# Optimization experiments

Measured on AMD Instinct MI355X. Metric: run time of the kernel, lower is better.

Reference implementation:

```python
import jax, jax.numpy as jnp
import numpy as np

N_NODES = 100000
N_FEAT = 512
HIDDEN = 64
N_CLASSES = 40
N_EDGES = 3200000
K = 10
ALPHA = 0.1


def setup_inputs() -> dict:
    key = jax.random.key(0)
    k1, k2, k3, k4 = jax.random.split(key, 4)
    x = jax.random.normal(k1, (N_NODES, N_FEAT), dtype=jnp.float32)
    # Glorot-ish scaled linear weights
    W1 = jax.random.normal(k2, (N_FEAT, HIDDEN), dtype=jnp.float32) / np.sqrt(N_FEAT)
    b1 = jnp.zeros((HIDDEN,), dtype=jnp.float32)
    W2 = jax.random.normal(k3, (HIDDEN, N_CLASSES), dtype=jnp.float32) / np.sqrt(HIDDEN)
    b2 = jnp.zeros((N_CLASSES,), dtype=jnp.float32)
    edge_index = jax.random.randint(k4, (2, N_EDGES), 0, N_NODES, dtype=jnp.int64)
    return {"x": x, "W1": W1, "b1": b1, "W2": W2, "b2": b2, "edge_index": edge_index}


def reference(x, W1, b1, W2, b2, edge_index):
    n = x.shape[0]
    # MLP (dropout is identity in eval mode)
    h = jnp.maximum(x @ W1 + b1, 0.0)
    h = h @ W2 + b2  # [N, C]

    # gcn_norm with self-loops: A_hat = D^{-1/2} (A + I) D^{-1/2}
    loops = jnp.arange(n, dtype=edge_index.dtype)
    row = jnp.concatenate([edge_index[0], loops])  # source (gather)
    col = jnp.concatenate([edge_index[1], loops])  # target (scatter)
    deg = jax.ops.segment_sum(jnp.ones(row.shape, dtype=h.dtype), col, num_segments=n)
    dinv = jnp.where(deg > 0, jax.lax.rsqrt(deg), 0.0)
    norm = dinv[row] * dinv[col]  # [E + N]

    h0 = h

    def step(z, _):
        msg = norm[:, None] * z[row]                      # gather + scale
        agg = jax.ops.segment_sum(msg, col, num_segments=n)  # scatter-add
        z = ALPHA * h0 + (1.0 - ALPHA) * agg
        return z, None

    z, _ = jax.lax.scan(step, h0, None, length=K)
    return jax.nn.log_softmax(z, axis=1)
```

## Files before the change

### kernel.cpp

```cpp
#include <hip/hip_runtime.h>
#include <hip/hip_bf16.h>
#include <hip/hip_fp16.h>

#define N_NODES   100000
#define N_FEAT    512
#define HIDDEN    64
#define N_CLASSES 40
#define KITER     10
#define ALPHA     0.1f
#define ZP        64
#define HPITCH    72
#define NXCD      8
#define WIN       (N_NODES / NXCD)
#define SUBCAP    65536
#define PARTB     2048
#define CAP       384

typedef __attribute__((ext_vector_type(8))) short bf16x8;
typedef __attribute__((ext_vector_type(4))) float f32x4;

__device__ __forceinline__ float bf2f(unsigned short u) {
    union { unsigned int i; float f; } c;
    c.i = ((unsigned int)u) << 16;
    return c.f;
}
__device__ __forceinline__ unsigned short f2bf(float f) {
    union { float f; unsigned int u; } c; c.f = f;
    unsigned int r = c.u + 0x7FFFu + ((c.u >> 16) & 1u);
    return (unsigned short)(r >> 16);
}

__global__ void zero_flags_kernel(int* __restrict__ flags) {
    if (threadIdx.x < 2) flags[threadIdx.x] = 0;
}

__global__ void detect_float_kernel(const unsigned short* __restrict__ w1raw,
                                    int* __restrict__ flags) {
    int i = blockIdx.x * blockDim.x + threadIdx.x;
    if (i < 32768) {
        unsigned short u = w1raw[i];
        if ((u & 0x7F80u) == 0x7F80u) atomicAdd(&flags[0], 1);
    }
}

__global__ void detect_edge_kernel(const int* __restrict__ ei, int* __restrict__ flags) {
    int i = blockIdx.x * blockDim.x + threadIdx.x;
    if (i < 2048) {
        if (ei[2 * i + 1] != 0) atomicAdd(&flags[1], 1);
    }
}

__global__ void pack_w1_kernel(const void* __restrict__ W1p, const int* __restrict__ flags,
                               unsigned short* __restrict__ pb) {
    int idx = blockIdx.x * 256 + threadIdx.x;
    int j    = idx & 7;
    int lane = (idx >> 3) & 63;
    int ktnt = idx >> 9;
    int kt = ktnt & 15, nt = ktnt >> 4;
    int k = kt * 32 + (lane >> 4) * 8 + j;
    int n = nt * 16 + (lane & 15);
    unsigned short v;
    if (flags[0] > 0) v = f2bf(((const float*)W1p)[k * HIDDEN + n]);
    else              v = ((const unsigned short*)W1p)[k * HIDDEN + n];
    pb[idx] = v;
}

__global__ void pack_w2_kernel(const void* __restrict__ W2p, const int* __restrict__ flags,
                               unsigned short* __restrict__ pb2) {
    int idx = blockIdx.x * 256 + threadIdx.x;
    if (idx >= 3072) return;
    int j    = idx & 7;
    int lane = (idx >> 3) & 63;
    int ktnt = idx >> 9;
    int kt = ktnt & 1, nt = ktnt >> 1;
    int k = kt * 32 + (lane >> 4) * 8 + j;
    int n = nt * 16 + (lane & 15);
    unsigned short v = 0;
    if (n < N_CLASSES) {
        if (flags[0] > 0) v = f2bf(((const float*)W2p)[k * N_CLASSES + n]);
        else              v = ((const unsigned short*)W2p)[k * N_CLASSES + n];
    }
    pb2[idx] = v;
}

__global__ __launch_bounds__(256) void mlp_kernel(
    const void* __restrict__ xp,
    const unsigned short* __restrict__ pb,
    const unsigned short* __restrict__ pb2,
    const void* __restrict__ b1p,
    const void* __restrict__ b2p,
    const int* __restrict__ flags,
    const float* __restrict__ dinv,
    float* __restrict__ h0,
    __half* __restrict__ zh0)
{
    __shared__ unsigned short hsb[16 * HPITCH];
    const int t    = threadIdx.x;
    const int wave = t >> 6;
    const int lane = t & 63;
    const int quad = lane >> 4;
    const int ml   = lane & 15;
    const int base = blockIdx.x * 16;
    const int isf32 = flags[0] > 0;

    const bf16x8* pbv = (const bf16x8*)pb;

    f32x4 acc = {0.f, 0.f, 0.f, 0.f};
    if (!isf32) {
        const unsigned short* xrow = (const unsigned short*)xp
                                   + (size_t)(base + ml) * N_FEAT + quad * 8;
        #pragma unroll
        for (int kt = 0; kt < 16; ++kt) {
            bf16x8 a = *(const bf16x8*)(xrow + kt * 32);
            bf16x8 b = pbv[(wave * 16 + kt) * 64 + lane];
            acc = __builtin_amdgcn_mfma_f32_16x16x32_bf16(a, b, acc, 0, 0, 0);
        }
    } else {
        const float* xf = (const float*)xp + (size_t)(base + ml) * N_FEAT + quad * 8;
        #pragma unroll
        for (int kt = 0; kt < 16; ++kt) {
            float4 lo = *(const float4*)(xf + kt * 32);
            float4 hi = *(const float4*)(xf + kt * 32 + 4);
            bf16x8 a;
            a[0] = (short)f2bf(lo.x); a[1] = (short)f2bf(lo.y);
            a[2] = (short)f2bf(lo.z); a[3] = (short)f2bf(lo.w);
            a[4] = (short)f2bf(hi.x); a[5] = (short)f2bf(hi.y);
            a[6] = (short)f2bf(hi.z); a[7] = (short)f2bf(hi.w);
            bf16x8 b = pbv[(wave * 16 + kt) * 64 + lane];
            acc = __builtin_amdgcn_mfma_f32_16x16x32_bf16(a, b, acc, 0, 0, 0);
        }
    }

    float b1v = isf32 ? ((const float*)b1p)[wave * 16 + ml]
                      : bf2f(((const unsigned short*)b1p)[wave * 16 + ml]);
    #pragma unroll
    for (int r = 0; r < 4; ++r)
        hsb[(quad * 4 + r) * HPITCH + wave * 16 + ml] = f2bf(fmaxf(acc[r] + b1v, 0.0f));
    __syncthreads();

    if (wave < 3) {
        const bf16x8* pb2v = (const bf16x8*)pb2;
        f32x4 acc2 = {0.f, 0.f, 0.f, 0.f};
        #pragma unroll
        for (int kt = 0; kt < 2; ++kt) {
            bf16x8 a = *(const bf16x8*)(hsb + ml * HPITCH + kt * 32 + quad * 8);
            bf16x8 b = pb2v[(wave * 2 + kt) * 64 + lane];
            acc2 = __builtin_amdgcn_mfma_f32_16x16x32_bf16(a, b, acc2, 0, 0, 0);
        }
        int n = wave * 16 + ml;
        if (n < N_CLASSES) {
            float b2v = isf32 ? ((const float*)b2p)[n] : bf2f(((const unsigned short*)b2p)[n]);
            #pragma unroll
            for (int r = 0; r < 4; ++r) {
                int node = base + quad * 4 + r;
                float v = acc2[r] + b2v;
                h0[(size_t)node * N_CLASSES + n] = v;
                zh0[(size_t)node * ZP + n] = __float2half(v * dinv[node]);
            }
        }
    }
}

__global__ void zero_cnt_kernel(int* __restrict__ cnt, int* __restrict__ cur) {
    int i = blockIdx.x * blockDim.x + threadIdx.x;
    if (i < N_NODES) cnt[i] = 0;
    if (i < 65) cur[i] = 0;
}

__global__ void dinv_kernel(const int* __restrict__ cnt, float* __restrict__ dinv) {
    int i = blockIdx.x * blockDim.x + threadIdx.x;
    if (i < N_NODES) dinv[i] = rsqrtf((float)cnt[i] + 1.0f);
}

__global__ void zero_pad_kernel(__half* __restrict__ a, __half* __restrict__ b) {
    int t = threadIdx.x;
    if (t < ZP)            a[(size_t)N_NODES * ZP + t]        = __float2half(0.0f);
    else if (t < 2 * ZP)   b[(size_t)N_NODES * ZP + (t - ZP)] = __float2half(0.0f);
}

__global__ __launch_bounds__(1024) void scan_kernel(
    const int* __restrict__ cnt, int* __restrict__ rptr, int* __restrict__ wpos, int E)
{
    __shared__ int wsum[16];
    __shared__ int carry_s, tiletot_s;
    const int t = threadIdx.x, wave = t >> 6, lane = t & 63;
    if (t == 0) carry_s = 0;
    __syncthreads();
    for (int base = 0; base < N_NODES; base += 4096) {
        int i0 = base + t * 4;
        int v0 = (i0 + 0 < N_NODES) ? cnt[i0 + 0] : 0;
        int v1 = (i0 + 1 < N_NODES) ? cnt[i0 + 1] : 0;
        int v2 = (i0 + 2 < N_NODES) ? cnt[i0 + 2] : 0;
        int v3 = (i0 + 3 < N_NODES) ? cnt[i0 + 3] : 0;
        int tl = v0 + v1 + v2 + v3;
        int sc = tl;
        #pragma unroll
        for (int off = 1; off < 64; off <<= 1) {
            int u = __shfl_up(sc, off, 64);
            if (lane >= off) sc += u;
        }
        if (lane == 63) wsum[wave] = sc;
        int wexcl = sc - tl;
        __syncthreads();
        if (wave == 0) {
            int wv = (lane < 16) ? wsum[lane] : 0;
            int ws = wv;
            #pragma unroll
            for (int off = 1; off < 16; off <<= 1) {
                int u = __shfl_up(ws, off, 64);
                if (lane >= off) ws += u;
            }
            if (lane < 16) wsum[lane] = ws - wv;
            if (lane == 15) tiletot_s = ws;
        }
        __syncthreads();
        int P  = carry_s + wsum[wave] + wexcl;
        int e0 = P, e1 = P + v0, e2 = e1 + v1, e3 = e2 + v2;
        if (i0 + 0 < N_NODES) { rptr[i0 + 0] = e0; wpos[i0 + 0] = e0; }
        if (i0 + 1 < N_NODES) { rptr[i0 + 1] = e1; wpos[i0 + 1] = e1; }
        if (i0 + 2 < N_NODES) { rptr[i0 + 2] = e2; wpos[i0 + 2] = e2; }
        if (i0 + 3 < N_NODES) { rptr[i0 + 3] = e3; wpos[i0 + 3] = e3; }
        __syncthreads();
        if (t == 0) carry_s += tiletot_s;
        __syncthreads();
    }
    if (t == 0) rptr[N_NODES] = E;
}

__global__ __launch_bounds__(256) void partition_kernel(
    const int* __restrict__ ei, const int* __restrict__ flags,
    int* __restrict__ cnt, unsigned int* __restrict__ sub,
    int* __restrict__ cur, int2* __restrict__ ovf, int E)
{
    __shared__ unsigned buf[NXCD][CAP];
    __shared__ int cnt_lds[NXCD];
    __shared__ unsigned base_s[NXCD];

    const int i64f = flags[1] == 0;
    const int xcd  = blockIdx.x & 7;
    const int per  = (E + PARTB - 1) / PARTB;
    const int e0   = blockIdx.x * per;
    const int e1   = min(e0 + per, E);

    if (threadIdx.x < NXCD) cnt_lds[threadIdx.x] = 0;
    __syncthreads();

    for (int e = e0 + threadIdx.x; e < e1; e += 256) {
        int c = i64f ? __builtin_nontemporal_load(ei + 2 * E + 2 * e)
                     : __builtin_nontemporal_load(ei + E + e);
        int r = i64f ? __builtin_nontemporal_load(ei + 2 * e)
                     : __builtin_nontemporal_load(ei + e);
        atomicAdd(&cnt[c], 1);
        int w = c / WIN;
        unsigned pk = (unsigned)r | ((unsigned)(c - w * WIN) << 17);
        int slot = atomicAdd(&cnt_lds[w], 1);
        if (slot < CAP) buf[w][slot] = pk;
        else { int op = atomicAdd(cur + 64, 1); ovf[op] = make_int2(r, c); }
    }
    __syncthreads();

    const int g   = threadIdx.x >> 5;
    const int l32 = threadIdx.x & 31;
    const int n   = min(cnt_lds[g], CAP);
    if (l32 == 0 && n > 0) base_s[g] = (unsigned)atomicAdd(&cur[g * 8 + xcd], n);
    __syncthreads();
    if (n > 0) {
        unsigned base = base_s[g];
        unsigned bslot = (unsigned)(g * 8 + xcd) * SUBCAP;
        for (int i = l32; i < n; i += 32) {
            unsigned p = base + (unsigned)i;
            unsigned pk = buf[g][i];
            if (p < SUBCAP) sub[bslot + p] = pk;
            else {
                int op = atomicAdd(cur + 64, 1);
                ovf[op] = make_int2((int)(pk & 0x1FFFFu), g * WIN + (int)(pk >> 17));
            }
        }
    }
}

__global__ __launch_bounds__(256) void scatter_kernel(
    const unsigned int* __restrict__ sub, const int* __restrict__ cur,
    const int2* __restrict__ ovf,
    int* __restrict__ wpos, int* __restrict__ srcidx)
{
    const int w = blockIdx.x & 7;
    const int tid64 = (blockIdx.x >> 3) * 256 + threadIdx.x;
    int P[9];
    P[0] = 0;
    #pragma unroll
    for (int a = 0; a < 8; ++a) {
        int na = cur[w * 8 + a];
        na = na > SUBCAP ? SUBCAP : na;
        P[a + 1] = P[a] + na;
    }
    const int total = P[8];
    for (int v = tid64; v < total; v += 65536) {
        int a = 0;
        #pragma unroll
        for (int q = 1; q < 8; ++q) if (v >= P[q]) a = q;
        unsigned pk = sub[(unsigned)(w * 8 + a) * SUBCAP + (v - P[a])];
        int r = (int)(pk & 0x1FFFFu);
        int c = w * WIN + (int)(pk >> 17);
        int pos = atomicAdd(&wpos[c], 1);
        srcidx[pos] = r;
    }
    int ov = cur[64];
    for (int i = tid64; i < ov; i += 65536) {
        int2 rc = ovf[i];
        if (rc.y / WIN == w) {
            int pos = atomicAdd(&wpos[rc.y], 1);
            srcidx[pos] = rc.x;
        }
    }
}

__global__ __launch_bounds__(256) void prop_kernel(
    const __half* __restrict__ zh, const float* __restrict__ h0,
    const float* __restrict__ dinv, const int* __restrict__ rptr,
    const int* __restrict__ srcidx, __half* __restrict__ zout)
{
    const int wave = threadIdx.x >> 6;
    const int lane = threadIdx.x & 63;
    const int g    = lane >> 4;
    const int l    = lane & 15;
    const int node = blockIdx.x * 16 + wave * 4 + g;
    const int c0   = l * 4;

    const int beg = rptr[node];
    const int end = rptr[node + 1];
    int nch = (end - beg + 15) >> 4;
    int m1    = max(nch, __shfl_xor(nch, 16, 64));
    int maxch = max(m1,  __shfl_xor(m1, 32, 64));

    float di = dinv[node];
    uint2 yself = *(const uint2*)(zh + ((size_t)node << 6) + c0);
    float h00 = 0.f, h01 = 0.f, h02 = 0.f, h03 = 0.f;
    if (c0 < N_CLASSES) {
        const float* hp = h0 + (size_t)node * N_CLASSES + c0;
        h00 = hp[0]; h01 = hp[1]; h02 = hp[2]; h03 = hp[3];
    }

    float a0 = 0.f, a1 = 0.f, a2 = 0.f, a3 = 0.f;
    float b0 = 0.f, b1 = 0.f, b2 = 0.f, b3 = 0.f;

    for (int ch = 0; ch < maxch; ++ch) {
        int idx = beg + ch * 16 + l;
        int sw  = (idx < end) ? srcidx[idx] : N_NODES;

        #pragma unroll
        for (int i = 0; i < 16; i += 2) {
            int s0 = __shfl(sw, (g << 4) + i,     64);
            int s1 = __shfl(sw, (g << 4) + i + 1, 64);
            uint2 z0 = *(const uint2*)(zh + ((size_t)s0 << 6) + c0);
            uint2 z1 = *(const uint2*)(zh + ((size_t)s1 << 6) + c0);
            const __half2* p0 = (const __half2*)&z0;
            const __half2* p1 = (const __half2*)&z1;
            float2 f00 = __half22float2(p0[0]);
            float2 f01 = __half22float2(p0[1]);
            float2 f10 = __half22float2(p1[0]);
            float2 f11 = __half22float2(p1[1]);
            a0 += f00.x; a1 += f00.y; a2 += f01.x; a3 += f01.y;
            b0 += f10.x; b1 += f10.y; b2 += f11.x; b3 += f11.y;
        }
    }

    if (c0 < N_CLASSES) {
        const __half2* ps = (const __half2*)&yself;
        float2 s01 = __half22float2(ps[0]);
        float2 s23 = __half22float2(ps[1]);
        float kk = (1.0f - ALPHA) * di;
        float o0 = ALPHA * h00 + kk * (a0 + b0 + s01.x);
        float o1 = ALPHA * h01 + kk * (a1 + b1 + s01.y);
        float o2 = ALPHA * h02 + kk * (a2 + b2 + s23.x);
        float o3 = ALPHA * h03 + kk * (a3 + b3 + s23.y);
        __half2 q01 = __floats2half2_rn(di * o0, di * o1);
        __half2 q23 = __floats2half2_rn(di * o2, di * o3);
        uint2 st;
        st.x = *(unsigned int*)&q01;
        st.y = *(unsigned int*)&q23;
        *(uint2*)(zout + ((size_t)node << 6) + c0) = st;
    }
}

__global__ __launch_bounds__(256) void lsm_kernel(
    const __half* __restrict__ zh, const float* __restrict__ dinv,
    const int* __restrict__ flags, void* __restrict__ outp)
{
    const int wave = threadIdx.x >> 6;
    const int lane = threadIdx.x & 63;
    const int node = blockIdx.x * 4 + wave;
    const int isf32 = flags[0] > 0;

    float di = dinv[node];
    float v = (lane < N_CLASSES)
            ? __half2float(zh[(size_t)node * ZP + lane]) / di : -1e30f;
    float m = v;
    #pragma unroll
    for (int o = 32; o; o >>= 1) m = fmaxf(m, __shfl_xor(m, o, 64));
    float e = (lane < N_CLASSES) ? expf(v - m) : 0.0f;
    float s = e;
    #pragma unroll
    for (int o = 32; o; o >>= 1) s += __shfl_xor(s, o, 64);
    float ls = logf(s);
    if (lane < N_CLASSES) {
        float r = v - m - ls;
        size_t idx = (size_t)node * N_CLASSES + lane;
        if (isf32) ((float*)outp)[idx] = r;
        else       ((__hip_bfloat16*)outp)[idx] = __float2bfloat16(r);
    }
}

extern "C" void kernel_launch(void* const* d_in, const int* in_sizes, int n_in,
                              void* d_out, int out_size, void* d_ws, size_t ws_size,
                              hipStream_t stream)
{
    const void* x  = d_in[0];
    const void* W1 = d_in[1];
    const void* b1 = d_in[2];
    const void* W2 = d_in[3];
    const void* b2 = d_in[4];
    const int* ei = (const int*)d_in[5];
    const int E = in_sizes[5] / 2;

    char* ws = (char*)d_ws;
    size_t off = 0;
    auto carve = [&](size_t bytes) -> void* {
        void* p = ws + off;
        off = (off + bytes + 255) & ~(size_t)255;
        return p;
    };
    float*  h0    = (float*) carve((size_t)N_NODES * N_CLASSES * 4);
    __half* zhA   = (__half*)carve((size_t)(N_NODES + 1) * ZP * 2);
    __half* zhB   = (__half*)carve((size_t)(N_NODES + 1) * ZP * 2);
    int*    cnt   = (int*)   carve((size_t)N_NODES * 4);
    float*  dinv  = (float*) carve((size_t)N_NODES * 4);
    int*    rptr  = (int*)   carve((size_t)(N_NODES + 1) * 4);
    int*    wpos  = (int*)   carve((size_t)N_NODES * 4);
    int*    srcidx= (int*)   carve((size_t)E * 4);
    unsigned int* sub = (unsigned int*)carve((size_t)64 * SUBCAP * 4);
    int*    cur   = (int*)   carve(65 * sizeof(int));
    unsigned short* pb  = (unsigned short*)carve(32768 * 2);
    unsigned short* pb2 = (unsigned short*)carve(3072 * 2);
    int*    flags = (int*)   carve(2 * sizeof(int));
    (void)ws_size; (void)n_in; (void)out_size;

    int2* ovf = (int2*)zhA;

    const int nodeBlocks = N_NODES / 4;
    const int mlpBlocks  = N_NODES / 16;
    const int propBlocks = N_NODES / 16;
    const int nThreads1  = (N_NODES + 255) / 256;

    zero_flags_kernel<<<1, 64, 0, stream>>>(flags);
    detect_float_kernel<<<128, 256, 0, stream>>>((const unsigned short*)W1, flags);
    detect_edge_kernel<<<8, 256, 0, stream>>>(ei, flags);
    pack_w1_kernel<<<128, 256, 0, stream>>>(W1, flags, pb);
    pack_w2_kernel<<<12, 256, 0, stream>>>(W2, flags, pb2);

    zero_cnt_kernel<<<nThreads1, 256, 0, stream>>>(cnt, cur);
    partition_kernel<<<PARTB, 256, 0, stream>>>(ei, flags, cnt, sub, cur, ovf, E);
    dinv_kernel<<<nThreads1, 256, 0, stream>>>(cnt, dinv);
    scan_kernel<<<1, 1024, 0, stream>>>(cnt, rptr, wpos, E);
    scatter_kernel<<<2048, 256, 0, stream>>>(sub, cur, ovf, wpos, srcidx);
    zero_pad_kernel<<<1, 128, 0, stream>>>(zhA, zhB);

    mlp_kernel<<<mlpBlocks, 256, 0, stream>>>(x, pb, pb2, b1, b2, flags, dinv, h0, zhA);

    const __half* zin = zhA;
    __half* zout = zhB;
    const __half* zlast = zhA;
    for (int it = 0; it < KITER; ++it) {
        prop_kernel<<<propBlocks, 256, 0, stream>>>(zin, h0, dinv, rptr, srcidx, zout);
        zlast = zout;
        zin = zout;
        zout = (zout == zhB) ? zhA : zhB;
    }

    lsm_kernel<<<nodeBlocks, 256, 0, stream>>>(zlast, dinv, flags, d_out);
}
```

Before: 1.250 ms.

## Replace global-atomic degree count and scatter with per-bucket LDS histograms

Drops the global atomicAdd on cnt in the partition pass. Degrees are now computed from per-subbucket LDS histograms of the packed edge buckets, and cnt_kernel reduces those histograms into cnt and dinv. The scatter pass uses LDS cursors seeded from rptr plus prefix histograms instead of global atomics on wpos. This trades millions of global atomics for an extra read pass over sub and only 64 blocks of 1024 threads, which may underuse the GPU in hist and scatter.

```diff
diff --git a/kernel.cpp b/kernel.cpp
--- a/kernel.cpp
+++ b/kernel.cpp
@@ -30,8 +30,10 @@
     return (unsigned short)(r >> 16);
 }
 
-__global__ void zero_flags_kernel(int* __restrict__ flags) {
-    if (threadIdx.x < 2) flags[threadIdx.x] = 0;
+__global__ void zero_cur_kernel(int* __restrict__ cur, int* __restrict__ flags) {
+    int t = threadIdx.x;
+    if (t < 65) cur[t] = 0;
+    if (t >= 65 && t < 67) flags[t - 65] = 0;
 }
 
 __global__ void detect_float_kernel(const unsigned short* __restrict__ w1raw,
@@ -161,25 +163,103 @@
     }
 }
 
-__global__ void zero_cnt_kernel(int* __restrict__ cnt, int* __restrict__ cur) {
-    int i = blockIdx.x * blockDim.x + threadIdx.x;
-    if (i < N_NODES) cnt[i] = 0;
-    if (i < 65) cur[i] = 0;
-}
-
-__global__ void dinv_kernel(const int* __restrict__ cnt, float* __restrict__ dinv) {
-    int i = blockIdx.x * blockDim.x + threadIdx.x;
-    if (i < N_NODES) dinv[i] = rsqrtf((float)cnt[i] + 1.0f);
-}
-
 __global__ void zero_pad_kernel(__half* __restrict__ a, __half* __restrict__ b) {
     int t = threadIdx.x;
     if (t < ZP)            a[(size_t)N_NODES * ZP + t]        = __float2half(0.0f);
     else if (t < 2 * ZP)   b[(size_t)N_NODES * ZP + (t - ZP)] = __float2half(0.0f);
 }
 
+__global__ __launch_bounds__(256) void partition_kernel(
+    const int* __restrict__ ei, const int* __restrict__ flags,
+    unsigned int* __restrict__ sub,
+    int* __restrict__ cur, int2* __restrict__ ovf, int E)
+{
+    __shared__ unsigned buf[NXCD][CAP];
+    __shared__ int cnt_lds[NXCD];
+    __shared__ unsigned base_s[NXCD];
+
+    const int i64f = flags[1] == 0;
+    const int xcd  = blockIdx.x & 7;
+    const int per  = (E + PARTB - 1) / PARTB;
+    const int e0   = blockIdx.x * per;
+    const int e1   = min(e0 + per, E);
+
+    if (threadIdx.x < NXCD) cnt_lds[threadIdx.x] = 0;
+    __syncthreads();
+
+    for (int e = e0 + threadIdx.x; e < e1; e += 256) {
+        int c = i64f ? __builtin_nontemporal_load(ei + 2 * E + 2 * e)
+                     : __builtin_nontemporal_load(ei + E + e);
+        int r = i64f ? __builtin_nontemporal_load(ei + 2 * e)
+                     : __builtin_nontemporal_load(ei + e);
+        int w = c / WIN;
+        unsigned pk = (unsigned)r | ((unsigned)(c - w * WIN) << 17);
+        int slot = atomicAdd(&cnt_lds[w], 1);
+        if (slot < CAP) buf[w][slot] = pk;
+        else { int op = atomicAdd(cur + 64, 1); ovf[op] = make_int2(r, c); }
+    }
+    __syncthreads();
+
+    const int g   = threadIdx.x >> 5;
+    const int l32 = threadIdx.x & 31;
+    const int n   = min(cnt_lds[g], CAP);
+    if (l32 == 0 && n > 0) base_s[g] = (unsigned)atomicAdd(&cur[g * 8 + xcd], n);
+    __syncthreads();
+    if (n > 0) {
+        unsigned base = base_s[g];
+        unsigned bslot = (unsigned)(g * 8 + xcd) * SUBCAP;
+        for (int i = l32; i < n; i += 32) {
+            unsigned p = base + (unsigned)i;
+            unsigned pk = buf[g][i];
+            if (p < SUBCAP) sub[bslot + p] = pk;
+            else {
+                int op = atomicAdd(cur + 64, 1);
+                ovf[op] = make_int2((int)(pk & 0x1FFFFu), g * WIN + (int)(pk >> 17));
+            }
+        }
+    }
+}
+
+__global__ __launch_bounds__(1024) void hist_kernel(
+    const unsigned int* __restrict__ sub, const int* __restrict__ cur,
+    const int2* __restrict__ ovf, int* __restrict__ hists)
+{
+    __shared__ int h[WIN];
+    const int w = blockIdx.x & 7;
+    const int s = blockIdx.x >> 3;
+    for (int off = threadIdx.x; off < WIN; off += 1024) h[off] = 0;
+    __syncthreads();
+    int n = min(cur[w * 8 + s], SUBCAP);
+    const unsigned int* sp = sub + (size_t)(w * 8 + s) * SUBCAP;
+    for (int i = threadIdx.x; i < n; i += 1024)
+        atomicAdd(&h[sp[i] >> 17], 1);
+    if (s == 7) {
+        int ov = cur[64];
+        for (int i = threadIdx.x; i < ov; i += 1024) {
+            int2 rc = ovf[i];
+            int ww = rc.y / WIN;
+            if (ww == w) atomicAdd(&h[rc.y - ww * WIN], 1);
+        }
+    }
+    __syncthreads();
+    for (int off = threadIdx.x; off < WIN; off += 1024)
+        hists[(size_t)(w * 8 + s) * WIN + off] = h[off];
+}
+
+__global__ void cnt_kernel(const int* __restrict__ hists, int* __restrict__ cnt,
+                           float* __restrict__ dinv) {
+    int i = blockIdx.x * 256 + threadIdx.x;
+    if (i >= N_NODES) return;
+    int w = i / WIN, off = i - w * WIN;
+    int c = 0;
+    #pragma unroll
+    for (int x = 0; x < 8; ++x) c += hists[(size_t)(w * 8 + x) * WIN + off];
+    cnt[i] = c;
+    dinv[i] = rsqrtf((float)c + 1.0f);
+}
+
 __global__ __launch_bounds__(1024) void scan_kernel(
-    const int* __restrict__ cnt, int* __restrict__ rptr, int* __restrict__ wpos, int E)
+    const int* __restrict__ cnt, int* __restrict__ rptr, int E)
 {
     __shared__ int wsum[16];
     __shared__ int carry_s, tiletot_s;
@@ -215,11 +295,10 @@
         }
         __syncthreads();
         int P  = carry_s + wsum[wave] + wexcl;
-        int e0 = P, e1 = P + v0, e2 = e1 + v1, e3 = e2 + v2;
-        if (i0 + 0 < N_NODES) { rptr[i0 + 0] = e0; wpos[i0 + 0] = e0; }
-        if (i0 + 1 < N_NODES) { rptr[i0 + 1] = e1; wpos[i0 + 1] = e1; }
-        if (i0 + 2 < N_NODES) { rptr[i0 + 2] = e2; wpos[i0 + 2] = e2; }
-        if (i0 + 3 < N_NODES) { rptr[i0 + 3] = e3; wpos[i0 + 3] = e3; }
+        if (i0 + 0 < N_NODES) rptr[i0 + 0] = P;
+        if (i0 + 1 < N_NODES) rptr[i0 + 1] = P + v0;
+        if (i0 + 2 < N_NODES) rptr[i0 + 2] = P + v0 + v1;
+        if (i0 + 3 < N_NODES) rptr[i0 + 3] = P + v0 + v1 + v2;
         __syncthreads();
         if (t == 0) carry_s += tiletot_s;
         __syncthreads();
@@ -227,90 +306,37 @@
     if (t == 0) rptr[N_NODES] = E;
 }
 
-__global__ __launch_bounds__(256) void partition_kernel(
-    const int* __restrict__ ei, const int* __restrict__ flags,
-    int* __restrict__ cnt, unsigned int* __restrict__ sub,
-    int* __restrict__ cur, int2* __restrict__ ovf, int E)
-{
-    __shared__ unsigned buf[NXCD][CAP];
-    __shared__ int cnt_lds[NXCD];
-    __shared__ unsigned base_s[NXCD];
-
-    const int i64f = flags[1] == 0;
-    const int xcd  = blockIdx.x & 7;
-    const int per  = (E + PARTB - 1) / PARTB;
-    const int e0   = blockIdx.x * per;
-    const int e1   = min(e0 + per, E);
-
-    if (threadIdx.x < NXCD) cnt_lds[threadIdx.x] = 0;
-    __syncthreads();
-
-    for (int e = e0 + threadIdx.x; e < e1; e += 256) {
-        int c = i64f ? __builtin_nontemporal_load(ei + 2 * E + 2 * e)
-                     : __builtin_nontemporal_load(ei + E + e);
-        int r = i64f ? __builtin_nontemporal_load(ei + 2 * e)
-                     : __builtin_nontemporal_load(ei + e);
-        atomicAdd(&cnt[c], 1);
-        int w = c / WIN;
-        unsigned pk = (unsigned)r | ((unsigned)(c - w * WIN) << 17);
-        int slot = atomicAdd(&cnt_lds[w], 1);
-        if (slot < CAP) buf[w][slot] = pk;
-        else { int op = atomicAdd(cur + 64, 1); ovf[op] = make_int2(r, c); }
-    }
-    __syncthreads();
-
-    const int g   = threadIdx.x >> 5;
-    const int l32 = threadIdx.x & 31;
-    const int n   = min(cnt_lds[g], CAP);
-    if (l32 == 0 && n > 0) base_s[g] = (unsigned)atomicAdd(&cur[g * 8 + xcd], n);
-    __syncthreads();
-    if (n > 0) {
-        unsigned base = base_s[g];
-        unsigned bslot = (unsigned)(g * 8 + xcd) * SUBCAP;
-        for (int i = l32; i < n; i += 32) {
-            unsigned p = base + (unsigned)i;
-            unsigned pk = buf[g][i];
-            if (p < SUBCAP) sub[bslot + p] = pk;
-            else {
-                int op = atomicAdd(cur + 64, 1);
-                ovf[op] = make_int2((int)(pk & 0x1FFFFu), g * WIN + (int)(pk >> 17));
+__global__ __launch_bounds__(1024) void scatter_kernel(
+    const unsigned int* __restrict__ sub, const int* __restrict__ cur,
+    const int* __restrict__ hists, const int2* __restrict__ ovf,
+    const int* __restrict__ rptr, int* __restrict__ srcidx)
+{
+    __shared__ int curs[WIN];
+    const int w = blockIdx.x & 7;
+    const int s = blockIdx.x >> 3;
+    for (int off = threadIdx.x; off < WIN; off += 1024) {
+        int base = rptr[w * WIN + off];
+        for (int x = 0; x < s; ++x)
+            base += hists[(size_t)(w * 8 + x) * WIN + off];
+        curs[off] = base;
+    }
+    __syncthreads();
+    int n = min(cur[w * 8 + s], SUBCAP);
+    const unsigned int* sp = sub + (size_t)(w * 8 + s) * SUBCAP;
+    for (int i = threadIdx.x; i < n; i += 1024) {
+        unsigned pk = sp[i];
+        int slot = atomicAdd(&curs[pk >> 17], 1);
+        srcidx[slot] = (int)(pk & 0x1FFFFu);
+    }
+    if (s == 7) {
+        int ov = cur[64];
+        for (int i = threadIdx.x; i < ov; i += 1024) {
+            int2 rc = ovf[i];
+            int ww = rc.y / WIN;
+            if (ww == w) {
+                int slot = atomicAdd(&curs[rc.y - ww * WIN], 1);
+                srcidx[slot] = rc.x;
             }
-        }
-    }
-}
-
-__global__ __launch_bounds__(256) void scatter_kernel(
-    const unsigned int* __restrict__ sub, const int* __restrict__ cur,
-    const int2* __restrict__ ovf,
-    int* __restrict__ wpos, int* __restrict__ srcidx)
-{
-    const int w = blockIdx.x & 7;
-    const int tid64 = (blockIdx.x >> 3) * 256 + threadIdx.x;
-    int P[9];
-    P[0] = 0;
-    #pragma unroll
-    for (int a = 0; a < 8; ++a) {
-        int na = cur[w * 8 + a];
-        na = na > SUBCAP ? SUBCAP : na;
-        P[a + 1] = P[a] + na;
-    }
-    const int total = P[8];
-    for (int v = tid64; v < total; v += 65536) {
-        int a = 0;
-        #pragma unroll
-        for (int q = 1; q < 8; ++q) if (v >= P[q]) a = q;
-        unsigned pk = sub[(unsigned)(w * 8 + a) * SUBCAP + (v - P[a])];
-        int r = (int)(pk & 0x1FFFFu);
-        int c = w * WIN + (int)(pk >> 17);
-        int pos = atomicAdd(&wpos[c], 1);
-        srcidx[pos] = r;
-    }
-    int ov = cur[64];
-    for (int i = tid64; i < ov; i += 65536) {
-        int2 rc = ovf[i];
-        if (rc.y / WIN == w) {
-            int pos = atomicAdd(&wpos[rc.y], 1);
-            srcidx[pos] = rc.x;
         }
     }
 }
@@ -436,9 +462,9 @@
     int*    cnt   = (int*)   carve((size_t)N_NODES * 4);
     float*  dinv  = (float*) carve((size_t)N_NODES * 4);
     int*    rptr  = (int*)   carve((size_t)(N_NODES + 1) * 4);
-    int*    wpos  = (int*)   carve((size_t)N_NODES * 4);
     int*    srcidx= (int*)   carve((size_t)E * 4);
     unsigned int* sub = (unsigned int*)carve((size_t)64 * SUBCAP * 4);
+    int*    hists = (int*)   carve((size_t)64 * WIN * 4);
     int*    cur   = (int*)   carve(65 * sizeof(int));
     unsigned short* pb  = (unsigned short*)carve(32768 * 2);
     unsigned short* pb2 = (unsigned short*)carve(3072 * 2);
@@ -450,19 +476,19 @@
     const int nodeBlocks = N_NODES / 4;
     const int mlpBlocks  = N_NODES / 16;
     const int propBlocks = N_NODES / 16;
-    const int nThreads1  = (N_NODES + 255) / 256;
-
-    zero_flags_kernel<<<1, 64, 0, stream>>>(flags);
+    const int cntBlocks  = (N_NODES + 255) / 256;
+
+    zero_cur_kernel<<<1, 128, 0, stream>>>(cur, flags);
     detect_float_kernel<<<128, 256, 0, stream>>>((const unsigned short*)W1, flags);
     detect_edge_kernel<<<8, 256, 0, stream>>>(ei, flags);
     pack_w1_kernel<<<128, 256, 0, stream>>>(W1, flags, pb);
     pack_w2_kernel<<<12, 256, 0, stream>>>(W2, flags, pb2);
 
-    zero_cnt_kernel<<<nThreads1, 256, 0, stream>>>(cnt, cur);
-    partition_kernel<<<PARTB, 256, 0, stream>>>(ei, flags, cnt, sub, cur, ovf, E);
-    dinv_kernel<<<nThreads1, 256, 0, stream>>>(cnt, dinv);
-    scan_kernel<<<1, 1024, 0, stream>>>(cnt, rptr, wpos, E);
-    scatter_kernel<<<2048, 256, 0, stream>>>(sub, cur, ovf, wpos, srcidx);
+    partition_kernel<<<PARTB, 256, 0, stream>>>(ei, flags, sub, cur, ovf, E);
+    hist_kernel<<<64, 1024, 0, stream>>>(sub, cur, ovf, hists);
+    cnt_kernel<<<cntBlocks, 256, 0, stream>>>(hists, cnt, dinv);
+    scan_kernel<<<1, 1024, 0, stream>>>(cnt, rptr, E);
+    scatter_kernel<<<64, 1024, 0, stream>>>(sub, cur, hists, ovf, rptr, srcidx);
     zero_pad_kernel<<<1, 128, 0, stream>>>(zhA, zhB);
 
     mlp_kernel<<<mlpBlocks, 256, 0, stream>>>(x, pb, pb2, b1, b2, flags, dinv, h0, zhA);
```

Measured after the change: 1.074 ms. -14.1%, faster.
